# Performance work log

Hardware: AMD Instinct MI355X
Metric: run time of the kernel (lower is better)

Reference implementation:

```python
import jax, jax.numpy as jnp
import numpy as np

ROUTING = 3
N_VERTEX = 32
D_CAP = 16
MULT_D = 64
B = 64
T_DIMS = {"text": 128, "audio": 512, "video": 256, "frames": 256}


def _xavier(key, shape):
    # torch xavier_normal_ on (T, n, MULT_d, d_c): receptive = MULT_d*d_c
    T, n, j, d = shape
    recep = j * d
    std = np.sqrt(2.0 / (n * recep + T * recep))
    return jax.random.normal(key, shape, dtype=jnp.float32) * std


def setup_inputs() -> dict:
    key = jax.random.key(0)
    ks = jax.random.split(key, 8)
    inp = {}
    for i, (name, T) in enumerate(T_DIMS.items()):
        inp[name] = jax.random.normal(ks[i], (B, T, MULT_D), dtype=jnp.float32)
    wnames = ["W_tpc", "W_apc", "W_vpc", "W_fpc"]
    for i, (name, (_, T)) in enumerate(zip(wnames, T_DIMS.items())):
        inp[name] = _xavier(ks[4 + i], (T, N_VERTEX, MULT_D, D_CAP))
    return inp


def _route(pri, routing):
    # pri: [B, T, n, d_c]; routing uses detached (stop-gradient) capsules
    pri_sg = jax.lax.stop_gradient(pri)
    Bn, T, n, d = pri.shape
    b = jnp.zeros((Bn, T, n), dtype=pri.dtype)
    for _ in range(routing):
        rc = jax.nn.softmax(b, axis=2)                      # [B, T, n]
        v = jnp.tanh(jnp.einsum('btnd,btn->bnd', pri_sg, rc))
        b = b + jnp.einsum('bnd,btnd->btn', v, pri_sg)      # agreement update
    rc = jnp.softmax(b, axis=2) if False else jax.nn.softmax(b, axis=2)
    # final vertex uses non-detached capsules with last routing coefficients
    return jnp.tanh(jnp.einsum('btnd,btn->bnd', pri, rc))


def reference(text, audio, video, frames, W_tpc, W_apc, W_vpc, W_fpc):
    outs = []
    for x, W in ((text, W_tpc), (audio, W_apc), (video, W_vpc), (frames, W_fpc)):
        pri = jnp.einsum('btj,tnjd->btnd', x, W)  # primary capsules [B,T,n,d_c]
        outs.append(_route(pri, ROUTING))
    return tuple(outs)
```

## Files before the change

### kernel.cpp

```cpp
#include <hip/hip_runtime.h>


typedef __attribute__((ext_vector_type(8))) short short8;
typedef __attribute__((ext_vector_type(4))) float floatx4;

static __device__ __forceinline__ unsigned short f2bf(float f) {
  union { float f; unsigned int i; } v;
  v.f = f;
  unsigned int x = v.i;
  return (unsigned short)((x + 0x7fffu + ((x >> 16) & 1u)) >> 16);
}

__global__ __launch_bounds__(256, 3) void pri_kernel(
    const float* __restrict__ x0, const float* __restrict__ x1,
    const float* __restrict__ x2, const float* __restrict__ x3,
    const float* __restrict__ w0, const float* __restrict__ w1,
    const float* __restrict__ w2, const float* __restrict__ w3,
    unsigned short* __restrict__ priAll) {
  __shared__ unsigned short wb[256 * 72];
  __shared__ unsigned short sc[4][16][136];

  int blk = blockIdx.x;
  int tid = threadIdx.x;

  int pair = blk >> 1, half = blk & 1;
  const float* x;
  const float* W;
  unsigned short* priM;
  int T, t0;
  if (pair < 64)       { x = x0; W = w0; priM = priAll;               T = 128; t0 = 2 * pair; }
  else if (pair < 320) { x = x1; W = w1; priM = priAll + 4194304ull;  T = 512; t0 = 2 * (pair - 64); }
  else if (pair < 448) { x = x2; W = w2; priM = priAll + 20971520ull; T = 256; t0 = 2 * (pair - 320); }
  else                 { x = x3; W = w3; priM = priAll + 29360128ull; T = 256; t0 = 2 * (pair - 448); }
  size_t TS = (size_t)T * 512;

  int lane = tid & 63, mt = tid >> 6;
  int m = lane & 15, q = lane >> 4;

  floatx4 xv[8];
  {
    const float* xrow = x + ((size_t)(mt * 16 + m) * T + t0) * 64;
#pragma unroll
    for (int tt = 0; tt < 2; ++tt)
#pragma unroll
      for (int s = 0; s < 2; ++s) {
        const floatx4* xp = (const floatx4*)(xrow + tt * 64 + s * 32 + q * 8);
        xv[tt * 4 + s * 2]     = __builtin_nontemporal_load(xp);
        xv[tt * 4 + s * 2 + 1] = __builtin_nontemporal_load(xp + 1);
      }
  }

  floatx4 wra[8], wrb[8];
  {
    const floatx4* Wf = (const floatx4*)(W + (size_t)t0 * 32768);
#pragma unroll
    for (int it = 0; it < 8; ++it) {
      int idx = it * 256 + tid;
      int nl = idx >> 7, jp = (idx >> 2) & 31, dq = idx & 3;
      int ng = half * 16 + nl;
      wra[it] = __builtin_nontemporal_load(Wf + ng * 256 + (2 * jp) * 4 + dq);
      wrb[it] = __builtin_nontemporal_load(Wf + ng * 256 + (2 * jp + 1) * 4 + dq);
    }
  }

  short8 afrag[2][2];
#pragma unroll
  for (int tt = 0; tt < 2; ++tt)
#pragma unroll
    for (int s = 0; s < 2; ++s) {
      floatx4 u0 = xv[tt * 4 + s * 2], u1 = xv[tt * 4 + s * 2 + 1];
      short8 a;
      a[0] = (short)f2bf(u0[0]); a[1] = (short)f2bf(u0[1]);
      a[2] = (short)f2bf(u0[2]); a[3] = (short)f2bf(u0[3]);
      a[4] = (short)f2bf(u1[0]); a[5] = (short)f2bf(u1[1]);
      a[6] = (short)f2bf(u1[2]); a[7] = (short)f2bf(u1[3]);
      afrag[tt][s] = a;
    }

  unsigned int* wb32 = (unsigned int*)wb;

#pragma unroll
  for (int it = 0; it < 8; ++it) {
    int idx = it * 256 + tid;
    int nl = idx >> 7, jp = (idx >> 2) & 31, dq = idx & 3;
    int rbase = nl * 16 + dq * 4;
#pragma unroll
    for (int k = 0; k < 4; ++k) {
      unsigned int dw = (unsigned int)f2bf(wra[it][k]) | ((unsigned int)f2bf(wrb[it][k]) << 16);
      wb32[(rbase + k) * 36 + jp] = dw;
    }
  }
  __syncthreads();

  {
    const floatx4* Wf = (const floatx4*)(W + (size_t)(t0 + 1) * 32768);
#pragma unroll
    for (int it = 0; it < 8; ++it) {
      int idx = it * 256 + tid;
      int nl = idx >> 7, jp = (idx >> 2) & 31, dq = idx & 3;
      int ng = half * 16 + nl;
      wra[it] = __builtin_nontemporal_load(Wf + ng * 256 + (2 * jp) * 4 + dq);
      wrb[it] = __builtin_nontemporal_load(Wf + ng * 256 + (2 * jp + 1) * 4 + dq);
    }
  }

  auto compute_t = [&](const short8& a0, const short8& a1, int t) {
    unsigned short* dst = priM + (size_t)t * 512 + half * 256;
    for (int g2 = 0; g2 < 2; ++g2) {
#pragma unroll
      for (int k = 0; k < 8; ++k) {
        int nt = g2 * 8 + k;
        const short8* b0p = (const short8*)&wb[(nt * 16 + m) * 72 + q * 8];
        const short8* b1p = (const short8*)&wb[(nt * 16 + m) * 72 + 32 + q * 8];
        short8 bf0 = *b0p, bf1 = *b1p;
        floatx4 acc = {0.f, 0.f, 0.f, 0.f};
        acc = __builtin_amdgcn_mfma_f32_16x16x32_bf16(a0, bf0, acc, 0, 0, 0);
        acc = __builtin_amdgcn_mfma_f32_16x16x32_bf16(a1, bf1, acc, 0, 0, 0);
#pragma unroll
        for (int reg = 0; reg < 4; ++reg)
          sc[mt][q * 4 + reg][k * 16 + m] = f2bf(acc[reg]);
      }
#pragma unroll
      for (int i = 0; i < 4; ++i) {
        int bl = (lane >> 4) + i * 4;
        int sh = (lane & 15) * 8;
        short8 v = *(const short8*)&sc[mt][bl][sh];
        *(short8*)(dst + (size_t)(mt * 16 + bl) * TS + g2 * 128 + sh) = v;
      }
    }
  };

  compute_t(afrag[0][0], afrag[0][1], t0);
  __syncthreads();

#pragma unroll
  for (int it = 0; it < 8; ++it) {
    int idx = it * 256 + tid;
    int nl = idx >> 7, jp = (idx >> 2) & 31, dq = idx & 3;
    int rbase = nl * 16 + dq * 4;
#pragma unroll
    for (int k = 0; k < 4; ++k) {
      unsigned int dw = (unsigned int)f2bf(wra[it][k]) | ((unsigned int)f2bf(wrb[it][k]) << 16);
      wb32[(rbase + k) * 36 + jp] = dw;
    }
  }
  __syncthreads();

  compute_t(afrag[1][0], afrag[1][1], t0 + 1);
}

__global__ __launch_bounds__(1024, 4) void route_kernel(
    const unsigned short* __restrict__ priAll, float* __restrict__ out) {
  __shared__ float Sl[32][640];
  __shared__ float Vc_s[544];

  int blk = blockIdx.x;
  int mod = blk & 3, b = blk >> 2;
  size_t poff; int T;
  if (mod == 0)      { poff = 0ull;         T = 128; }
  else if (mod == 1) { poff = 4194304ull;   T = 512; }
  else if (mod == 2) { poff = 20971520ull;  T = 256; }
  else               { poff = 29360128ull;  T = 256; }

  const unsigned short* priM = priAll + poff + (size_t)b * T * 512;

  int tid = threadIdx.x;
  int n = tid & 31, g = tid >> 5;
  int nbase = n * 17;

  if (tid < 544) Vc_s[tid] = 0.f;
  __syncthreads();

  int iters = T >> 5;

  for (int pass = 0; pass < 4; ++pass) {
    float Vc[16];
#pragma unroll
    for (int d = 0; d < 16; ++d) Vc[d] = Vc_s[nbase + d];

    float acc[16];
#pragma unroll
    for (int d = 0; d < 16; ++d) acc[d] = 0.f;

    const uint4* pr = (const uint4*)(priM + (size_t)g * 512 + n * 16);
    uint4 ca = pr[0], cb = pr[1];
    uint4 na = pr[2048], nb = pr[2049];

    for (int it = 0; it < iters; ++it) {
      int poffu = (it + 2 < iters) ? 4096 : 0;
      uint4 fa = pr[poffu], fb = pr[poffu + 1];

      float p[16];
      {
        unsigned int wds[8] = {ca.x, ca.y, ca.z, ca.w, cb.x, cb.y, cb.z, cb.w};
#pragma unroll
        for (int k = 0; k < 8; ++k) {
          union { unsigned int u; float f; } lo, hi;
          lo.u = wds[k] << 16;
          hi.u = wds[k] & 0xffff0000u;
          p[2 * k] = lo.f;
          p[2 * k + 1] = hi.f;
        }
      }
      float logit = 0.f;
#pragma unroll
      for (int d = 0; d < 16; ++d) logit += p[d] * Vc[d];
      float e = __expf(logit);
      float s = e;
#pragma unroll
      for (int o = 16; o >= 1; o >>= 1) s += __shfl_xor(s, o, 32);
      float rc = e / s;
#pragma unroll
      for (int d = 0; d < 16; ++d) acc[d] += rc * p[d];

      asm volatile("" :: "v"(fa.x), "v"(fa.y), "v"(fa.z), "v"(fa.w),
                         "v"(fb.x), "v"(fb.y), "v"(fb.z), "v"(fb.w));

      ca = na; cb = nb; na = fa; nb = fb;
      pr += 2048;
    }

#pragma unroll
    for (int d = 0; d < 16; ++d) Sl[g][nbase + d] = acc[d];
    __syncthreads();

    if (tid < 512) {
      int nn = tid >> 4, dd = tid & 15;
      int idx = nn * 17 + dd;
      float s = 0.f;
#pragma unroll
      for (int gg = 0; gg < 32; ++gg) s += Sl[gg][idx];
      float v = tanhf(s);
      if (pass == 3) out[(size_t)(mod * 64 + b) * 512 + tid] = v;
      else Vc_s[idx] += v;
    }
    __syncthreads();
  }
}

extern "C" void kernel_launch(void* const* d_in, const int* in_sizes, int n_in,
                              void* d_out, int out_size, void* d_ws, size_t ws_size,
                              hipStream_t stream) {
  const float* x0 = (const float*)d_in[0];
  const float* x1 = (const float*)d_in[1];
  const float* x2 = (const float*)d_in[2];
  const float* x3 = (const float*)d_in[3];
  const float* w0 = (const float*)d_in[4];
  const float* w1 = (const float*)d_in[5];
  const float* w2 = (const float*)d_in[6];
  const float* w3 = (const float*)d_in[7];

  unsigned short* pri = (unsigned short*)d_ws;

  pri_kernel<<<1152, 256, 0, stream>>>(x0, x1, x2, x3, w0, w1, w2, w3, pri);
  route_kernel<<<256, 1024, 0, stream>>>(pri, (float*)d_out);
}
```

Baseline: 243.5 us.

## Cache routing capsule rows in registers and LDS across routing passes

```diff
diff --git a/kernel.cpp b/kernel.cpp
--- a/kernel.cpp
+++ b/kernel.cpp
@@ -151,7 +151,8 @@
 
 __global__ __launch_bounds__(1024, 4) void route_kernel(
     const unsigned short* __restrict__ priAll, float* __restrict__ out) {
-  __shared__ float Sl[32][640];
+  __shared__ unsigned short Ld[96 * 528];
+  __shared__ float Sl[16][544];
   __shared__ float Vc_s[544];
 
   int blk = blockIdx.x;
@@ -166,33 +167,87 @@
 
   int tid = threadIdx.x;
   int n = tid & 31, g = tid >> 5;
+  int wv = tid >> 6;
   int nbase = n * 17;
+  int R = T >> 5;
+  int nlds = (R >= 6) ? 3 : (R - 3);
+  int nglob = (R > 6) ? (R - 6) : 0;
 
   if (tid < 544) Vc_s[tid] = 0.f;
   __syncthreads();
 
-  int iters = T >> 5;
-
-  for (int pass = 0; pass < 4; ++pass) {
+  const uint4* base = (const uint4*)(priM + (size_t)g * 512 + n * 16);
+
+  float acc[16];
+  uint4 r0a, r0b, r1a, r1b, r2a, r2b;
+
+  auto accum_row = [&](uint4 a, uint4 c) {
+    unsigned int wds[8] = {a.x, a.y, a.z, a.w, c.x, c.y, c.z, c.w};
+#pragma unroll
+    for (int k = 0; k < 8; ++k) {
+      union { unsigned int u; float f; } lo, hi;
+      lo.u = wds[k] << 16;
+      hi.u = wds[k] & 0xffff0000u;
+      acc[2 * k]     += lo.f;
+      acc[2 * k + 1] += hi.f;
+    }
+  };
+
+  auto epilogue = [&](int pass) {
+#pragma unroll
+    for (int d = 0; d < 16; ++d) acc[d] += __shfl_xor(acc[d], 32, 64);
+    if ((tid & 63) < 32) {
+#pragma unroll
+      for (int d = 0; d < 16; ++d) Sl[wv][nbase + d] = acc[d];
+    }
+    __syncthreads();
+    if (tid < 512) {
+      int idx = (tid >> 4) * 17 + (tid & 15);
+      float s = 0.f;
+#pragma unroll
+      for (int w = 0; w < 16; ++w) s += Sl[w][idx];
+      float v = tanhf(s);
+      if (pass == 3) out[(size_t)(mod * 64 + b) * 512 + tid] = v;
+      else Vc_s[idx] += v;
+    }
+    __syncthreads();
+  };
+
+#pragma unroll
+  for (int d = 0; d < 16; ++d) acc[d] = 0.f;
+
+  r0a = base[0];    r0b = base[1];
+  r1a = base[2048]; r1b = base[2049];
+  r2a = base[4096]; r2b = base[4097];
+  accum_row(r0a, r0b);
+  accum_row(r1a, r1b);
+  accum_row(r2a, r2b);
+
+  for (int i = 0; i < nlds; ++i) {
+    uint4 a = base[(3 + i) * 2048], c = base[(3 + i) * 2048 + 1];
+    uint4* ldp = (uint4*)&Ld[(i * 32 + g) * 528 + n * 16];
+    ldp[0] = a; ldp[1] = c;
+    accum_row(a, c);
+  }
+  for (int i = 0; i < nglob; ++i) {
+    uint4 a = base[(6 + i) * 2048], c = base[(6 + i) * 2048 + 1];
+    accum_row(a, c);
+  }
+#pragma unroll
+  for (int d = 0; d < 16; ++d) acc[d] *= 0.03125f;
+  epilogue(0);
+
+  for (int pass = 1; pass < 4; ++pass) {
     float Vc[16];
 #pragma unroll
     for (int d = 0; d < 16; ++d) Vc[d] = Vc_s[nbase + d];
-
-    float acc[16];
 #pragma unroll
     for (int d = 0; d < 16; ++d) acc[d] = 0.f;
 
-    const uint4* pr = (const uint4*)(priM + (size_t)g * 512 + n * 16);
-    uint4 ca = pr[0], cb = pr[1];
-    uint4 na = pr[2048], nb = pr[2049];
-
-    for (int it = 0; it < iters; ++it) {
-      int poffu = (it + 2 < iters) ? 4096 : 0;
-      uint4 fa = pr[poffu], fb = pr[poffu + 1];
-
+    auto proc_row = [&](uint4 a, uint4 c) {
       float p[16];
       {
-        unsigned int wds[8] = {ca.x, ca.y, ca.z, ca.w, cb.x, cb.y, cb.z, cb.w};
+        unsigned int wds[8] = {a.x, a.y, a.z, a.w, c.x, c.y, c.z, c.w};
 #pragma unroll
         for (int k = 0; k < 8; ++k) {
           union { unsigned int u; float f; } lo, hi;
@@ -212,29 +267,20 @@
       float rc = e / s;
 #pragma unroll
       for (int d = 0; d < 16; ++d) acc[d] += rc * p[d];
-
-      asm volatile("" :: "v"(fa.x), "v"(fa.y), "v"(fa.z), "v"(fa.w),
-                         "v"(fb.x), "v"(fb.y), "v"(fb.z), "v"(fb.w));
-
-      ca = na; cb = nb; na = fa; nb = fb;
-      pr += 2048;
-    }
-
-#pragma unroll
-    for (int d = 0; d < 16; ++d) Sl[g][nbase + d] = acc[d];
-    __syncthreads();
-
-    if (tid < 512) {
-      int nn = tid >> 4, dd = tid & 15;
-      int idx = nn * 17 + dd;
-      float s = 0.f;
-#pragma unroll
-      for (int gg = 0; gg < 32; ++gg) s += Sl[gg][idx];
-      float v = tanhf(s);
-      if (pass == 3) out[(size_t)(mod * 64 + b) * 512 + tid] = v;
-      else Vc_s[idx] += v;
-    }
-    __syncthreads();
+    };
+
+    proc_row(r0a, r0b);
+    proc_row(r1a, r1b);
+    proc_row(r2a, r2b);
+    for (int i = 0; i < nlds; ++i) {
+      const uint4* ldp = (const uint4*)&Ld[(i * 32 + g) * 528 + n * 16];
+      proc_row(ldp[0], ldp[1]);
+    }
+    for (int i = 0; i < nglob; ++i) {
+      uint4 a = base[(6 + i) * 2048], c = base[(6 + i) * 2048 + 1];
+      proc_row(a, c);
+    }
+    epilogue(pass);
   }
 }
 
```

Result: faster. 236.3 us (-3.0%).
